# Optimization experiments

Measured on AMD Instinct MI355X. Metric: run time of the kernel, lower is better.

Reference implementation:

```python
import jax, jax.numpy as jnp
import numpy as np

NQ, NKV, D = 32, 8, 64
HID = 2048
EPS = 1e-5
THETA = 1000000.0


def _rmsnorm(x, w):
    var = jnp.mean(x * x, axis=-1, keepdims=True)
    return x * jax.lax.rsqrt(var + EPS) * w


def setup_inputs() -> dict:
    key = jax.random.key(0)
    k1, k2, k3 = jax.random.split(key, 3)
    T = 2048
    positions = jnp.arange(T, dtype=jnp.int64) if jax.config.jax_enable_x64 else jnp.arange(T, dtype=jnp.int32)
    hidden_states = jax.random.normal(k1, (T, HID), dtype=jnp.float32)
    w_qkv = jax.random.normal(k2, (HID, (NQ + 2 * NKV) * D), dtype=jnp.float32) / np.sqrt(HID)
    w_out = jax.random.normal(k3, (NQ * D, HID), dtype=jnp.float32) / np.sqrt(NQ * D)
    q_ln_w = jnp.ones((D,), dtype=jnp.float32)
    k_ln_w = jnp.ones((D,), dtype=jnp.float32)
    return {"positions": positions, "hidden_states": hidden_states, "w_qkv": w_qkv,
            "w_out": w_out, "q_ln_w": q_ln_w, "k_ln_w": k_ln_w}


def reference(positions, hidden_states, w_qkv, w_out, q_ln_w, k_ln_w):
    T = hidden_states.shape[0]
    qkv = hidden_states @ w_qkv  # [T, (NQ+2*NKV)*D]
    q = qkv[:, : NQ * D].reshape(T, NQ, D)
    k = qkv[:, NQ * D : (NQ + NKV) * D].reshape(T, NKV, D)
    v = qkv[:, (NQ + NKV) * D :].reshape(T, NKV, D)
    # per-head RMSNorm on q and k
    q = _rmsnorm(q, q_ln_w)
    k = _rmsnorm(k, k_ln_w)
    # neox-style RoPE (rotate halves)
    inv_freq = 1.0 / (THETA ** (jnp.arange(0, D, 2, dtype=jnp.float32) / D))
    ang = positions.astype(jnp.float32)[:, None] * inv_freq  # [T, D/2]
    cos = jnp.cos(ang)[:, None, :]
    sin = jnp.sin(ang)[:, None, :]
    def rope(x):
        x1, x2 = x[..., : D // 2], x[..., D // 2 :]
        return jnp.concatenate([x1 * cos - x2 * sin, x2 * cos + x1 * sin], axis=-1)
    q = rope(q)
    k = rope(k)
    # grouped-query causal attention (one sequence, positions define order)
    G = NQ // NKV
    qg = q.reshape(T, NKV, G, D)
    scores = jnp.einsum('tkgd,skd->kgts', qg, k) * (D ** -0.5)  # [NKV,G,T,T]
    causal = jnp.arange(T)[:, None] >= jnp.arange(T)[None, :]
    scores = jnp.where(causal[None, None], scores, -1e30)
    probs = jax.nn.softmax(scores, axis=-1)
    attn = jnp.einsum('kgts,skd->tkgd', probs, v).reshape(T, NQ * D)
    return attn @ w_out
```

## Files before the change

kernel.cpp:

```cpp
#include <hip/hip_runtime.h>

typedef __bf16 bhalf;
typedef __bf16 bhalf8 __attribute__((ext_vector_type(8)));
typedef __bf16 bhalf4 __attribute__((ext_vector_type(4)));
typedef float f32x4 __attribute__((ext_vector_type(4)));

typedef __attribute__((address_space(1))) const void* gas_p;
typedef __attribute__((address_space(3))) void* las_p;

#define T_SEQ 2048
#define HIDN  2048
#define NQH   32
#define NKVH  8
#define DH    64
#define NQKV  3072

__global__ __launch_bounds__(256) void cast_bf16_k(const float* __restrict__ in,
                                                   bhalf* __restrict__ out, int n) {
  int i = (blockIdx.x * 256 + threadIdx.x) * 4;
  if (i + 3 < n) {
    float4 v = *(const float4*)(in + i);
    bhalf4 o;
    o[0] = (bhalf)v.x; o[1] = (bhalf)v.y; o[2] = (bhalf)v.z; o[3] = (bhalf)v.w;
    *(bhalf4*)(out + i) = o;
  }
}

__global__ __launch_bounds__(256) void transpose_cast_k(const float* __restrict__ in,
                                                        bhalf* __restrict__ out, int R, int C) {
  __shared__ float tile[32][33];
  int bx = blockIdx.x * 32;
  int by = blockIdx.y * 32;
  int tx = threadIdx.x & 31, ty = threadIdx.x >> 5;
#pragma unroll
  for (int p = 0; p < 4; ++p)
    tile[ty + 8 * p][tx] = in[(size_t)(by + ty + 8 * p) * C + bx + tx];
  __syncthreads();
#pragma unroll
  for (int p = 0; p < 4; ++p)
    out[(size_t)(bx + ty + 8 * p) * R + by + tx] = (bhalf)tile[tx][ty + 8 * p];
}

__global__ __launch_bounds__(256) void transpose_bf16_k(const bhalf* __restrict__ in,
                                                        bhalf* __restrict__ out, int R, int C) {
  __shared__ bhalf tile[32][33];
  int bx = blockIdx.x * 32;
  int by = blockIdx.y * 32;
  int tx = threadIdx.x & 31, ty = threadIdx.x >> 5;
#pragma unroll
  for (int p = 0; p < 4; ++p)
    tile[ty + 8 * p][tx] = in[(size_t)(by + ty + 8 * p) * C + bx + tx];
  __syncthreads();
#pragma unroll
  for (int p = 0; p < 4; ++p)
    out[(size_t)(bx + ty + 8 * p) * R + by + tx] = tile[tx][ty + 8 * p];
}

__device__ __forceinline__ void gemm_core(const bhalf* __restrict__ A,
                                          const bhalf* __restrict__ Bt, int K,
                                          int bm, int bn, int tid,
                                          bhalf* As, bhalf* Bs, f32x4 acc[2][4]) {
  int lane = tid & 63, wv = tid >> 6;
  int m16 = lane & 15, q4 = lane >> 4;
  int srow = tid >> 3;
  int scol = ((tid & 7) ^ (srow & 7)) * 8;
  const bhalf* asrc = A + (size_t)(bm + srow) * K + scol;
  const bhalf* bsrc = Bt + (size_t)(bn + srow) * K + scol;
  bhalf* adst = As + (wv * 8) * 64;
  bhalf* bdst = Bs + (wv * 8) * 64;
  int swz = m16 & 7;

  for (int k0 = 0; k0 < K; k0 += 64) {
#pragma unroll
    for (int c = 0; c < 4; ++c)
      __builtin_amdgcn_global_load_lds((gas_p)(asrc + (size_t)(c * 32) * K + k0),
                                       (las_p)(adst + c * 2048), 16, 0, 0);
#pragma unroll
    for (int c = 0; c < 2; ++c)
      __builtin_amdgcn_global_load_lds((gas_p)(bsrc + (size_t)(c * 32) * K + k0),
                                       (las_p)(bdst + c * 2048), 16, 0, 0);
    __syncthreads();
    bhalf8 af[2][2], bf[4][2];
#pragma unroll
    for (int mi = 0; mi < 2; ++mi)
#pragma unroll
      for (int ks = 0; ks < 2; ++ks)
        af[mi][ks] = *(const bhalf8*)&As[(wv * 32 + mi * 16 + m16) * 64 +
                                         (((ks * 4 + q4) ^ swz) * 8)];
#pragma unroll
    for (int ni = 0; ni < 4; ++ni)
#pragma unroll
      for (int ks = 0; ks < 2; ++ks)
        bf[ni][ks] = *(const bhalf8*)&Bs[(ni * 16 + m16) * 64 +
                                         (((ks * 4 + q4) ^ swz) * 8)];
#pragma unroll
    for (int mi = 0; mi < 2; ++mi)
#pragma unroll
      for (int ni = 0; ni < 4; ++ni) {
        acc[mi][ni] = __builtin_amdgcn_mfma_f32_16x16x32_bf16(af[mi][0], bf[ni][0], acc[mi][ni], 0, 0, 0);
        acc[mi][ni] = __builtin_amdgcn_mfma_f32_16x16x32_bf16(af[mi][1], bf[ni][1], acc[mi][ni], 0, 0, 0);
      }
    __syncthreads();
  }
}

__global__ __launch_bounds__(256) void gemm1_fused_k(const bhalf* __restrict__ A,
                                                     const bhalf* __restrict__ Bt,
                                                     const int* __restrict__ pos,
                                                     const float* __restrict__ qw,
                                                     const float* __restrict__ kw,
                                                     bhalf* __restrict__ qo,
                                                     bhalf* __restrict__ ko,
                                                     bhalf* __restrict__ vo) {
  __shared__ __align__(16) bhalf As[128 * 64];
  __shared__ __align__(16) bhalf Bs[64 * 64];
  int tid = threadIdx.x, lane = tid & 63, wv = tid >> 6;
  int m16 = lane & 15, q4 = lane >> 4;
  int bm = blockIdx.y * 128, bn = blockIdx.x * 64, h = blockIdx.x;
  f32x4 zero4 = {0.f, 0.f, 0.f, 0.f};
  f32x4 acc[2][4];
#pragma unroll
  for (int mi = 0; mi < 2; ++mi)
#pragma unroll
    for (int ni = 0; ni < 4; ++ni) acc[mi][ni] = zero4;

  gemm_core(A, Bt, HIDN, bm, bn, tid, As, Bs, acc);

  int wr0 = wv * 32;
  if (h < 40) {
    float wd[4];
    const float* wptr = (h < 32) ? qw : kw;
#pragma unroll
    for (int ni = 0; ni < 4; ++ni) wd[ni] = wptr[ni * 16 + m16];
    float f0 = exp2f((float)m16 * -0.6228615177913804f);
    float f1 = f0 * 0.001f;
#pragma unroll
    for (int mi = 0; mi < 2; ++mi)
#pragma unroll
      for (int r = 0; r < 4; ++r) {
        int trow = bm + wr0 + mi * 16 + q4 * 4 + r;
        float x0 = acc[mi][0][r], x1 = acc[mi][1][r], x2 = acc[mi][2][r], x3 = acc[mi][3][r];
        float ss = x0 * x0 + x1 * x1 + x2 * x2 + x3 * x3;
        ss += __shfl_xor(ss, 1);
        ss += __shfl_xor(ss, 2);
        ss += __shfl_xor(ss, 4);
        ss += __shfl_xor(ss, 8);
        float sc = rsqrtf(ss * (1.0f / 64.0f) + 1e-5f);
        float y0 = x0 * sc * wd[0], y1 = x1 * sc * wd[1];
        float y2 = x2 * sc * wd[2], y3 = x3 * sc * wd[3];
        float p = (float)pos[trow];
        float a0 = p * f0, a1 = p * f1;
        float c0 = cosf(a0), s0 = sinf(a0), c1 = cosf(a1), s1 = sinf(a1);
        float o0 = y0 * c0 - y2 * s0, o2 = y2 * c0 + y0 * s0;
        float o1 = y1 * c1 - y3 * s1, o3 = y3 * c1 + y1 * s1;
        bhalf* dst = (h < 32) ? (qo + (size_t)trow * 2048 + h * 64 + m16)
                              : (ko + (size_t)trow * 512 + (h - 32) * 64 + m16);
        dst[0] = (bhalf)o0; dst[16] = (bhalf)o1; dst[32] = (bhalf)o2; dst[48] = (bhalf)o3;
      }
  } else {
#pragma unroll
    for (int mi = 0; mi < 2; ++mi)
#pragma unroll
      for (int r = 0; r < 4; ++r) {
        int trow = bm + wr0 + mi * 16 + q4 * 4 + r;
        bhalf* dst = vo + (size_t)trow * 512 + (h - 40) * 64 + m16;
        dst[0] = (bhalf)acc[mi][0][r]; dst[16] = (bhalf)acc[mi][1][r];
        dst[32] = (bhalf)acc[mi][2][r]; dst[48] = (bhalf)acc[mi][3][r];
      }
  }
}

__global__ __launch_bounds__(256) void gemm2_k(const bhalf* __restrict__ A,
                                               const bhalf* __restrict__ Bt,
                                               float* __restrict__ C) {
  __shared__ __align__(16) bhalf As[128 * 64];
  __shared__ __align__(16) bhalf Bs[64 * 64];
  int tid = threadIdx.x, lane = tid & 63, wv = tid >> 6;
  int m16 = lane & 15, q4 = lane >> 4;
  int bm = blockIdx.y * 128, bn = blockIdx.x * 64;
  f32x4 zero4 = {0.f, 0.f, 0.f, 0.f};
  f32x4 acc[2][4];
#pragma unroll
  for (int mi = 0; mi < 2; ++mi)
#pragma unroll
    for (int ni = 0; ni < 4; ++ni) acc[mi][ni] = zero4;

  gemm_core(A, Bt, HIDN, bm, bn, tid, As, Bs, acc);

  int wr0 = wv * 32;
#pragma unroll
  for (int mi = 0; mi < 2; ++mi)
#pragma unroll
    for (int r = 0; r < 4; ++r) {
      size_t base = (size_t)(bm + wr0 + mi * 16 + q4 * 4 + r) * 2048 + bn + m16;
      C[base] = acc[mi][0][r]; C[base + 16] = acc[mi][1][r];
      C[base + 32] = acc[mi][2][r]; C[base + 48] = acc[mi][3][r];
    }
}

__global__ __launch_bounds__(256) void attn_k(const bhalf* __restrict__ q,
                                              const bhalf* __restrict__ k,
                                              const bhalf* __restrict__ vt,
                                              bhalf* __restrict__ o) {
  __shared__ __align__(16) bhalf Kb[2][4096];
  __shared__ __align__(16) bhalf Vb[2][4096];
  __shared__ __align__(16) bhalf Pb[4][16][72];
  int tid = threadIdx.x, lane = tid & 63, w = tid >> 6;
  int h = blockIdx.x, kh = h >> 2;
  int qt = 31 - blockIdx.y;
  int qb = qt * 64;
  int m16 = lane & 15, q4 = lane >> 4;
  int wrow0 = qb + w * 16;

  const float C1 = 0.18033688011112042f;
  const float C2 = 11.541560327111707f;

  const bhalf* qp = q + (size_t)(wrow0 + m16) * 2048 + h * 64;
  bhalf8 qf0 = *(const bhalf8*)(qp + q4 * 8);
  bhalf8 qf1 = *(const bhalf8*)(qp + 32 + q4 * 8);

  int srow = tid >> 3;
  int scol = ((tid & 7) ^ (srow & 7)) * 8;
  const bhalf* ksrc = k + (size_t)srow * 512 + kh * 64 + scol;
  const bhalf* vsrc = vt + (size_t)(kh * 64 + srow) * 2048 + scol;
  bhalf* kdst = &Kb[0][0] + w * 512;
  bhalf* vdst = &Vb[0][0] + w * 512;

  auto stage = [&](int c) {
    int buf = c & 1, s0 = c * 64;
#pragma unroll
    for (int j = 0; j < 2; ++j) {
      __builtin_amdgcn_global_load_lds((gas_p)(ksrc + (size_t)(s0 + j * 32) * 512),
                                       (las_p)(kdst + buf * 4096 + j * 2048), 16, 0, 0);
      __builtin_amdgcn_global_load_lds((gas_p)(vsrc + (size_t)(j * 32) * 2048 + s0),
                                       (las_p)(vdst + buf * 4096 + j * 2048), 16, 0, 0);
    }
  };

  f32x4 zero4 = {0.f, 0.f, 0.f, 0.f};
  f32x4 oac[4];
  float psum[4] = {0.f, 0.f, 0.f, 0.f};
#pragma unroll
  for (int ni = 0; ni < 4; ++ni) oac[ni] = zero4;
  int swz = m16 & 7;

  stage(0);
  for (int c = 0; c <= qt; ++c) {
    __syncthreads();
    if (c < qt) stage(c + 1);
    int buf = c & 1, s0 = c * 64;
    if (c < qt) {
      bhalf8 kf[4][2];
#pragma unroll
      for (int st = 0; st < 4; ++st)
#pragma unroll
        for (int ks = 0; ks < 2; ++ks)
          kf[st][ks] = *(const bhalf8*)&Kb[buf][(st * 16 + m16) * 64 + (((ks * 4 + q4) ^ swz) * 8)];
      f32x4 sv[4];
#pragma unroll
      for (int st = 0; st < 4; ++st) {
        f32x4 t0 = __builtin_amdgcn_mfma_f32_16x16x32_bf16(qf0, kf[st][0], zero4, 0, 0, 0);
        sv[st] = __builtin_amdgcn_mfma_f32_16x16x32_bf16(qf1, kf[st][1], t0, 0, 0, 0);
      }
#pragma unroll
      for (int st = 0; st < 4; ++st)
#pragma unroll
        for (int r = 0; r < 4; ++r) {
          float pe = exp2f(sv[st][r] * C1 - C2);
          psum[r] += pe;
          Pb[w][q4 * 4 + r][st * 16 + m16] = (bhalf)pe;
        }
      bhalf8 vf[4][2];
#pragma unroll
      for (int ni = 0; ni < 4; ++ni)
#pragma unroll
        for (int ks = 0; ks < 2; ++ks)
          vf[ni][ks] = *(const bhalf8*)&Vb[buf][(ni * 16 + m16) * 64 + (((ks * 4 + q4) ^ swz) * 8)];
      bhalf8 ap0 = *(const bhalf8*)&Pb[w][m16][q4 * 8];
      bhalf8 ap1 = *(const bhalf8*)&Pb[w][m16][32 + q4 * 8];
#pragma unroll
      for (int ni = 0; ni < 4; ++ni) {
        oac[ni] = __builtin_amdgcn_mfma_f32_16x16x32_bf16(ap0, vf[ni][0], oac[ni], 0, 0, 0);
        oac[ni] = __builtin_amdgcn_mfma_f32_16x16x32_bf16(ap1, vf[ni][1], oac[ni], 0, 0, 0);
      }
    } else {
      bhalf8 kf[4][2];
      f32x4 sv[4];
#pragma unroll
      for (int st = 0; st < 4; ++st)
        if (st <= w) {
#pragma unroll
          for (int ks = 0; ks < 2; ++ks)
            kf[st][ks] = *(const bhalf8*)&Kb[buf][(st * 16 + m16) * 64 + (((ks * 4 + q4) ^ swz) * 8)];
          f32x4 t0 = __builtin_amdgcn_mfma_f32_16x16x32_bf16(qf0, kf[st][0], zero4, 0, 0, 0);
          sv[st] = __builtin_amdgcn_mfma_f32_16x16x32_bf16(qf1, kf[st][1], t0, 0, 0, 0);
        }
      int stwr = (w >= 2) ? 3 : 1;
#pragma unroll
      for (int st = 0; st < 4; ++st) {
        if (st > stwr) continue;
#pragma unroll
        for (int r = 0; r < 4; ++r) {
          float pe = 0.f;
          if (st <= w) {
            int trow = wrow0 + q4 * 4 + r;
            int col = s0 + st * 16 + m16;
            pe = (col <= trow) ? exp2f(sv[st][r] * C1 - C2) : 0.f;
          }
          psum[r] += pe;
          Pb[w][q4 * 4 + r][st * 16 + m16] = (bhalf)pe;
        }
      }
      int ksmax = (w >= 2) ? 1 : 0;
      bhalf8 vf[4][2];
#pragma unroll
      for (int ni = 0; ni < 4; ++ni)
#pragma unroll
        for (int ks = 0; ks < 2; ++ks)
          if (ks <= ksmax)
            vf[ni][ks] = *(const bhalf8*)&Vb[buf][(ni * 16 + m16) * 64 + (((ks * 4 + q4) ^ swz) * 8)];
      bhalf8 ap0 = *(const bhalf8*)&Pb[w][m16][q4 * 8];
#pragma unroll
      for (int ni = 0; ni < 4; ++ni)
        oac[ni] = __builtin_amdgcn_mfma_f32_16x16x32_bf16(ap0, vf[ni][0], oac[ni], 0, 0, 0);
      if (ksmax) {
        bhalf8 ap1 = *(const bhalf8*)&Pb[w][m16][32 + q4 * 8];
#pragma unroll
        for (int ni = 0; ni < 4; ++ni)
          oac[ni] = __builtin_amdgcn_mfma_f32_16x16x32_bf16(ap1, vf[ni][1], oac[ni], 0, 0, 0);
      }
    }
  }
#pragma unroll
  for (int r = 0; r < 4; ++r) {
    float ps = psum[r];
    ps += __shfl_xor(ps, 1);
    ps += __shfl_xor(ps, 2);
    ps += __shfl_xor(ps, 4);
    ps += __shfl_xor(ps, 8);
    psum[r] = 1.0f / ps;
  }
#pragma unroll
  for (int ni = 0; ni < 4; ++ni)
#pragma unroll
    for (int r = 0; r < 4; ++r) {
      int trow = wrow0 + q4 * 4 + r;
      o[(size_t)trow * 2048 + h * 64 + ni * 16 + m16] = (bhalf)(oac[ni][r] * psum[r]);
    }
}

extern "C" void kernel_launch(void* const* d_in, const int* in_sizes, int n_in,
                              void* d_out, int out_size, void* d_ws, size_t ws_size,
                              hipStream_t stream) {
  const int* positions = (const int*)d_in[0];
  const float* hidden  = (const float*)d_in[1];
  const float* w_qkv   = (const float*)d_in[2];
  const float* w_out   = (const float*)d_in[3];
  const float* q_ln    = (const float*)d_in[4];
  const float* k_ln    = (const float*)d_in[5];
  float* out = (float*)d_out;

  char* wsp = (char*)d_ws;
  bhalf* hid_bf  = (bhalf*)(wsp);
  bhalf* wqkvT   = (bhalf*)(wsp + 8388608);
  bhalf* woutT   = (bhalf*)(wsp + 20971520);
  bhalf* q_bf    = (bhalf*)(wsp + 29360128);
  bhalf* k_bf    = (bhalf*)(wsp + 37748736);
  bhalf* v_bf    = (bhalf*)(wsp + 39845888);
  bhalf* vt_g    = (bhalf*)(wsp + 41943040);
  bhalf* attn_bf = (bhalf*)(wsp + 44040192);

  cast_bf16_k<<<T_SEQ * HIDN / 1024, 256, 0, stream>>>(hidden, hid_bf, T_SEQ * HIDN);
  transpose_cast_k<<<dim3(NQKV / 32, HIDN / 32), 256, 0, stream>>>(w_qkv, wqkvT, HIDN, NQKV);
  transpose_cast_k<<<dim3(HIDN / 32, HIDN / 32), 256, 0, stream>>>(w_out, woutT, HIDN, HIDN);
  gemm1_fused_k<<<dim3(NQKV / 64, T_SEQ / 128), 256, 0, stream>>>(
      hid_bf, wqkvT, positions, q_ln, k_ln, q_bf, k_bf, v_bf);
  transpose_bf16_k<<<dim3(512 / 32, T_SEQ / 32), 256, 0, stream>>>(v_bf, vt_g, T_SEQ, 512);
  attn_k<<<dim3(NQH, 32), 256, 0, stream>>>(q_bf, k_bf, vt_g, attn_bf);
  gemm2_k<<<dim3(HIDN / 64, T_SEQ / 128), 256, 0, stream>>>(attn_bf, woutT, out);
}
```

Before: 222.7 us.

## Widen attention query tiles, split-K output GEMM, vectorize weight transpose-cast

The attention kernel now gives each block 128 query rows and each wave 32 rows in two MFMA row tiles, so every staged K/V chunk is reused across twice as many queries. The diagonal-chunk masking is recomputed for the new tiling, and the kernel gets a launch-bounds occupancy hint. The output projection GEMM is split into two K halves, which doubles the grid to fill more CUs, and a new elementwise kernel sums the two partial results, at the cost of extra fp32 traffic and one more launch. The weight transpose-casts now use 64x64 tiles with float4 loads and 16-byte bf16 stores, and the workspace layout is reshuffled so the partial buffers alias the dead inputs.

```diff
diff --git a/kernel.cpp b/kernel.cpp
--- a/kernel.cpp
+++ b/kernel.cpp
@@ -26,19 +26,28 @@
   }
 }
 
-__global__ __launch_bounds__(256) void transpose_cast_k(const float* __restrict__ in,
-                                                        bhalf* __restrict__ out, int R, int C) {
-  __shared__ float tile[32][33];
-  int bx = blockIdx.x * 32;
-  int by = blockIdx.y * 32;
-  int tx = threadIdx.x & 31, ty = threadIdx.x >> 5;
-#pragma unroll
-  for (int p = 0; p < 4; ++p)
-    tile[ty + 8 * p][tx] = in[(size_t)(by + ty + 8 * p) * C + bx + tx];
+__global__ __launch_bounds__(256) void transpose_cast64_k(const float* __restrict__ in,
+                                                          bhalf* __restrict__ out,
+                                                          int R, int C) {
+  __shared__ bhalf tile[64][72];
+  int tid = threadIdx.x;
+  int bx = blockIdx.x * 64;
+  int by = blockIdx.y * 64;
+  int rl = tid >> 4, c4 = (tid & 15) * 4;
+#pragma unroll
+  for (int p = 0; p < 4; ++p) {
+    float4 v = *(const float4*)(in + (size_t)(by + rl + 16 * p) * C + bx + c4);
+    bhalf4 b;
+    b[0] = (bhalf)v.x; b[1] = (bhalf)v.y; b[2] = (bhalf)v.z; b[3] = (bhalf)v.w;
+    *(bhalf4*)&tile[rl + 16 * p][c4] = b;
+  }
   __syncthreads();
-#pragma unroll
-  for (int p = 0; p < 4; ++p)
-    out[(size_t)(bx + ty + 8 * p) * R + by + tx] = (bhalf)tile[tx][ty + 8 * p];
+  int c = tid >> 2, r0 = (tid & 3) * 16;
+  bhalf8 o0, o1;
+#pragma unroll
+  for (int j = 0; j < 8; ++j) { o0[j] = tile[r0 + j][c]; o1[j] = tile[r0 + 8 + j][c]; }
+  *(bhalf8*)(out + (size_t)(bx + c) * R + by + r0) = o0;
+  *(bhalf8*)(out + (size_t)(bx + c) * R + by + r0 + 8) = o1;
 }
 
 __global__ __launch_bounds__(256) void transpose_bf16_k(const bhalf* __restrict__ in,
@@ -57,27 +66,28 @@
 }
 
 __device__ __forceinline__ void gemm_core(const bhalf* __restrict__ A,
-                                          const bhalf* __restrict__ Bt, int K,
+                                          const bhalf* __restrict__ Bt,
+                                          int Kstride, int Klen,
                                           int bm, int bn, int tid,
                                           bhalf* As, bhalf* Bs, f32x4 acc[2][4]) {
   int lane = tid & 63, wv = tid >> 6;
   int m16 = lane & 15, q4 = lane >> 4;
   int srow = tid >> 3;
   int scol = ((tid & 7) ^ (srow & 7)) * 8;
-  const bhalf* asrc = A + (size_t)(bm + srow) * K + scol;
-  const bhalf* bsrc = Bt + (size_t)(bn + srow) * K + scol;
+  const bhalf* asrc = A + (size_t)(bm + srow) * Kstride + scol;
+  const bhalf* bsrc = Bt + (size_t)(bn + srow) * Kstride + scol;
   bhalf* adst = As + (wv * 8) * 64;
   bhalf* bdst = Bs + (wv * 8) * 64;
   int swz = m16 & 7;
 
-  for (int k0 = 0; k0 < K; k0 += 64) {
+  for (int k0 = 0; k0 < Klen; k0 += 64) {
 #pragma unroll
     for (int c = 0; c < 4; ++c)
-      __builtin_amdgcn_global_load_lds((gas_p)(asrc + (size_t)(c * 32) * K + k0),
+      __builtin_amdgcn_global_load_lds((gas_p)(asrc + (size_t)(c * 32) * Kstride + k0),
                                        (las_p)(adst + c * 2048), 16, 0, 0);
 #pragma unroll
     for (int c = 0; c < 2; ++c)
-      __builtin_amdgcn_global_load_lds((gas_p)(bsrc + (size_t)(c * 32) * K + k0),
+      __builtin_amdgcn_global_load_lds((gas_p)(bsrc + (size_t)(c * 32) * Kstride + k0),
                                        (las_p)(bdst + c * 2048), 16, 0, 0);
     __syncthreads();
     bhalf8 af[2][2], bf[4][2];
@@ -124,7 +134,7 @@
 #pragma unroll
     for (int ni = 0; ni < 4; ++ni) acc[mi][ni] = zero4;
 
-  gemm_core(A, Bt, HIDN, bm, bn, tid, As, Bs, acc);
+  gemm_core(A, Bt, HIDN, HIDN, bm, bn, tid, As, Bs, acc);
 
   int wr0 = wv * 32;
   if (h < 40) {
@@ -172,12 +182,13 @@
 
 __global__ __launch_bounds__(256) void gemm2_k(const bhalf* __restrict__ A,
                                                const bhalf* __restrict__ Bt,
-                                               float* __restrict__ C) {
+                                               float* __restrict__ Cpart) {
   __shared__ __align__(16) bhalf As[128 * 64];
   __shared__ __align__(16) bhalf Bs[64 * 64];
   int tid = threadIdx.x, lane = tid & 63, wv = tid >> 6;
   int m16 = lane & 15, q4 = lane >> 4;
   int bm = blockIdx.y * 128, bn = blockIdx.x * 64;
+  int slice = blockIdx.z;
   f32x4 zero4 = {0.f, 0.f, 0.f, 0.f};
   f32x4 acc[2][4];
 #pragma unroll
@@ -185,8 +196,9 @@
 #pragma unroll
     for (int ni = 0; ni < 4; ++ni) acc[mi][ni] = zero4;
 
-  gemm_core(A, Bt, HIDN, bm, bn, tid, As, Bs, acc);
-
+  gemm_core(A + slice * 1024, Bt + slice * 1024, HIDN, 1024, bm, bn, tid, As, Bs, acc);
+
+  float* C = Cpart + (size_t)slice * (T_SEQ * HIDN);
   int wr0 = wv * 32;
 #pragma unroll
   for (int mi = 0; mi < 2; ++mi)
@@ -198,26 +210,43 @@
     }
 }
 
-__global__ __launch_bounds__(256) void attn_k(const bhalf* __restrict__ q,
-                                              const bhalf* __restrict__ k,
-                                              const bhalf* __restrict__ vt,
-                                              bhalf* __restrict__ o) {
+__global__ __launch_bounds__(256) void add2_k(const float* __restrict__ p0,
+                                              const float* __restrict__ p1,
+                                              float* __restrict__ out) {
+  int i = (blockIdx.x * 256 + threadIdx.x) * 4;
+  float4 a = *(const float4*)(p0 + i);
+  float4 b = *(const float4*)(p1 + i);
+  float4 o = {a.x + b.x, a.y + b.y, a.z + b.z, a.w + b.w};
+  *(float4*)(out + i) = o;
+}
+
+__global__ __launch_bounds__(256, 3) void attn_k(const bhalf* __restrict__ q,
+                                                 const bhalf* __restrict__ k,
+                                                 const bhalf* __restrict__ vt,
+                                                 bhalf* __restrict__ o) {
   __shared__ __align__(16) bhalf Kb[2][4096];
   __shared__ __align__(16) bhalf Vb[2][4096];
-  __shared__ __align__(16) bhalf Pb[4][16][72];
+  __shared__ __align__(16) bhalf Pb[4][32][72];
   int tid = threadIdx.x, lane = tid & 63, w = tid >> 6;
   int h = blockIdx.x, kh = h >> 2;
-  int qt = 31 - blockIdx.y;
-  int qb = qt * 64;
+  int qt = 15 - blockIdx.y;
+  int qb = qt * 128;
   int m16 = lane & 15, q4 = lane >> 4;
-  int wrow0 = qb + w * 16;
+  int wrow0 = qb + w * 32;
+  int dw = w & 1;
+  int c_d = wrow0 >> 6;
+  int nch = 2 * qt + 2;
 
   const float C1 = 0.18033688011112042f;
   const float C2 = 11.541560327111707f;
 
-  const bhalf* qp = q + (size_t)(wrow0 + m16) * 2048 + h * 64;
-  bhalf8 qf0 = *(const bhalf8*)(qp + q4 * 8);
-  bhalf8 qf1 = *(const bhalf8*)(qp + 32 + q4 * 8);
+  bhalf8 qf[2][2];
+#pragma unroll
+  for (int mt = 0; mt < 2; ++mt) {
+    const bhalf* qp = q + (size_t)(wrow0 + mt * 16 + m16) * 2048 + h * 64;
+    qf[mt][0] = *(const bhalf8*)(qp + q4 * 8);
+    qf[mt][1] = *(const bhalf8*)(qp + 32 + q4 * 8);
+  }
 
   int srow = tid >> 3;
   int scol = ((tid & 7) ^ (srow & 7)) * 8;
@@ -238,115 +267,138 @@
   };
 
   f32x4 zero4 = {0.f, 0.f, 0.f, 0.f};
-  f32x4 oac[4];
-  float psum[4] = {0.f, 0.f, 0.f, 0.f};
-#pragma unroll
-  for (int ni = 0; ni < 4; ++ni) oac[ni] = zero4;
+  f32x4 oac[2][4];
+  float psum[2][4];
+#pragma unroll
+  for (int mt = 0; mt < 2; ++mt)
+#pragma unroll
+    for (int ni = 0; ni < 4; ++ni) oac[mt][ni] = zero4;
+#pragma unroll
+  for (int mt = 0; mt < 2; ++mt)
+#pragma unroll
+    for (int r = 0; r < 4; ++r) psum[mt][r] = 0.f;
   int swz = m16 & 7;
 
   stage(0);
-  for (int c = 0; c <= qt; ++c) {
+  for (int c = 0; c < nch; ++c) {
     __syncthreads();
-    if (c < qt) stage(c + 1);
-    int buf = c & 1, s0 = c * 64;
-    if (c < qt) {
+    if (c + 1 < nch) stage(c + 1);
+    if (c > c_d) continue;
+    int buf = c & 1;
+    if (c < c_d) {
       bhalf8 kf[4][2];
 #pragma unroll
       for (int st = 0; st < 4; ++st)
 #pragma unroll
         for (int ks = 0; ks < 2; ++ks)
           kf[st][ks] = *(const bhalf8*)&Kb[buf][(st * 16 + m16) * 64 + (((ks * 4 + q4) ^ swz) * 8)];
-      f32x4 sv[4];
-#pragma unroll
-      for (int st = 0; st < 4; ++st) {
-        f32x4 t0 = __builtin_amdgcn_mfma_f32_16x16x32_bf16(qf0, kf[st][0], zero4, 0, 0, 0);
-        sv[st] = __builtin_amdgcn_mfma_f32_16x16x32_bf16(qf1, kf[st][1], t0, 0, 0, 0);
-      }
-#pragma unroll
-      for (int st = 0; st < 4; ++st)
-#pragma unroll
-        for (int r = 0; r < 4; ++r) {
-          float pe = exp2f(sv[st][r] * C1 - C2);
-          psum[r] += pe;
-          Pb[w][q4 * 4 + r][st * 16 + m16] = (bhalf)pe;
+#pragma unroll
+      for (int mt = 0; mt < 2; ++mt) {
+        f32x4 sv[4];
+#pragma unroll
+        for (int st = 0; st < 4; ++st) {
+          f32x4 t0 = __builtin_amdgcn_mfma_f32_16x16x32_bf16(qf[mt][0], kf[st][0], zero4, 0, 0, 0);
+          sv[st] = __builtin_amdgcn_mfma_f32_16x16x32_bf16(qf[mt][1], kf[st][1], t0, 0, 0, 0);
         }
+#pragma unroll
+        for (int st = 0; st < 4; ++st)
+#pragma unroll
+          for (int r = 0; r < 4; ++r) {
+            float pe = exp2f(sv[st][r] * C1 - C2);
+            psum[mt][r] += pe;
+            Pb[w][mt * 16 + q4 * 4 + r][st * 16 + m16] = (bhalf)pe;
+          }
+      }
       bhalf8 vf[4][2];
 #pragma unroll
       for (int ni = 0; ni < 4; ++ni)
 #pragma unroll
         for (int ks = 0; ks < 2; ++ks)
           vf[ni][ks] = *(const bhalf8*)&Vb[buf][(ni * 16 + m16) * 64 + (((ks * 4 + q4) ^ swz) * 8)];
-      bhalf8 ap0 = *(const bhalf8*)&Pb[w][m16][q4 * 8];
-      bhalf8 ap1 = *(const bhalf8*)&Pb[w][m16][32 + q4 * 8];
-#pragma unroll
-      for (int ni = 0; ni < 4; ++ni) {
-        oac[ni] = __builtin_amdgcn_mfma_f32_16x16x32_bf16(ap0, vf[ni][0], oac[ni], 0, 0, 0);
-        oac[ni] = __builtin_amdgcn_mfma_f32_16x16x32_bf16(ap1, vf[ni][1], oac[ni], 0, 0, 0);
+#pragma unroll
+      for (int mt = 0; mt < 2; ++mt) {
+        bhalf8 ap0 = *(const bhalf8*)&Pb[w][mt * 16 + m16][q4 * 8];
+        bhalf8 ap1 = *(const bhalf8*)&Pb[w][mt * 16 + m16][32 + q4 * 8];
+#pragma unroll
+        for (int ni = 0; ni < 4; ++ni) {
+          oac[mt][ni] = __builtin_amdgcn_mfma_f32_16x16x32_bf16(ap0, vf[ni][0], oac[mt][ni], 0, 0, 0);
+          oac[mt][ni] = __builtin_amdgcn_mfma_f32_16x16x32_bf16(ap1, vf[ni][1], oac[mt][ni], 0, 0, 0);
+        }
       }
     } else {
+      int stwr = 1 + 2 * dw;
       bhalf8 kf[4][2];
-      f32x4 sv[4];
 #pragma unroll
       for (int st = 0; st < 4; ++st)
-        if (st <= w) {
+        if (st <= stwr)
 #pragma unroll
           for (int ks = 0; ks < 2; ++ks)
             kf[st][ks] = *(const bhalf8*)&Kb[buf][(st * 16 + m16) * 64 + (((ks * 4 + q4) ^ swz) * 8)];
-          f32x4 t0 = __builtin_amdgcn_mfma_f32_16x16x32_bf16(qf0, kf[st][0], zero4, 0, 0, 0);
-          sv[st] = __builtin_amdgcn_mfma_f32_16x16x32_bf16(qf1, kf[st][1], t0, 0, 0, 0);
+#pragma unroll
+      for (int mt = 0; mt < 2; ++mt) {
+        f32x4 sv[4];
+#pragma unroll
+        for (int st = 0; st < 4; ++st)
+          if (st <= mt + 2 * dw) {
+            f32x4 t0 = __builtin_amdgcn_mfma_f32_16x16x32_bf16(qf[mt][0], kf[st][0], zero4, 0, 0, 0);
+            sv[st] = __builtin_amdgcn_mfma_f32_16x16x32_bf16(qf[mt][1], kf[st][1], t0, 0, 0, 0);
+          }
+#pragma unroll
+        for (int st = 0; st < 4; ++st) {
+          if (st > stwr) continue;
+          int d = st - 2 * dw - mt;
+#pragma unroll
+          for (int r = 0; r < 4; ++r) {
+            float pe = 0.f;
+            if (d < 0) pe = exp2f(sv[st][r] * C1 - C2);
+            else if (d == 0) pe = (m16 <= q4 * 4 + r) ? exp2f(sv[st][r] * C1 - C2) : 0.f;
+            psum[mt][r] += pe;
+            Pb[w][mt * 16 + q4 * 4 + r][st * 16 + m16] = (bhalf)pe;
+          }
         }
-      int stwr = (w >= 2) ? 3 : 1;
-#pragma unroll
-      for (int st = 0; st < 4; ++st) {
-        if (st > stwr) continue;
-#pragma unroll
-        for (int r = 0; r < 4; ++r) {
-          float pe = 0.f;
-          if (st <= w) {
-            int trow = wrow0 + q4 * 4 + r;
-            int col = s0 + st * 16 + m16;
-            pe = (col <= trow) ? exp2f(sv[st][r] * C1 - C2) : 0.f;
-          }
-          psum[r] += pe;
-          Pb[w][q4 * 4 + r][st * 16 + m16] = (bhalf)pe;
+      }
+      bhalf8 vf[4][2];
+#pragma unroll
+      for (int ni = 0; ni < 4; ++ni) {
+        vf[ni][0] = *(const bhalf8*)&Vb[buf][(ni * 16 + m16) * 64 + ((q4 ^ swz) * 8)];
+        if (dw)
+          vf[ni][1] = *(const bhalf8*)&Vb[buf][(ni * 16 + m16) * 64 + (((4 + q4) ^ swz) * 8)];
+      }
+#pragma unroll
+      for (int mt = 0; mt < 2; ++mt) {
+        bhalf8 ap0 = *(const bhalf8*)&Pb[w][mt * 16 + m16][q4 * 8];
+#pragma unroll
+        for (int ni = 0; ni < 4; ++ni)
+          oac[mt][ni] = __builtin_amdgcn_mfma_f32_16x16x32_bf16(ap0, vf[ni][0], oac[mt][ni], 0, 0, 0);
+        if (dw) {
+          bhalf8 ap1 = *(const bhalf8*)&Pb[w][mt * 16 + m16][32 + q4 * 8];
+#pragma unroll
+          for (int ni = 0; ni < 4; ++ni)
+            oac[mt][ni] = __builtin_amdgcn_mfma_f32_16x16x32_bf16(ap1, vf[ni][1], oac[mt][ni], 0, 0, 0);
         }
       }
-      int ksmax = (w >= 2) ? 1 : 0;
-      bhalf8 vf[4][2];
-#pragma unroll
-      for (int ni = 0; ni < 4; ++ni)
-#pragma unroll
-        for (int ks = 0; ks < 2; ++ks)
-          if (ks <= ksmax)
-            vf[ni][ks] = *(const bhalf8*)&Vb[buf][(ni * 16 + m16) * 64 + (((ks * 4 + q4) ^ swz) * 8)];
-      bhalf8 ap0 = *(const bhalf8*)&Pb[w][m16][q4 * 8];
-#pragma unroll
-      for (int ni = 0; ni < 4; ++ni)
-        oac[ni] = __builtin_amdgcn_mfma_f32_16x16x32_bf16(ap0, vf[ni][0], oac[ni], 0, 0, 0);
-      if (ksmax) {
-        bhalf8 ap1 = *(const bhalf8*)&Pb[w][m16][32 + q4 * 8];
-#pragma unroll
-        for (int ni = 0; ni < 4; ++ni)
-          oac[ni] = __builtin_amdgcn_mfma_f32_16x16x32_bf16(ap1, vf[ni][1], oac[ni], 0, 0, 0);
-      }
     }
   }
 #pragma unroll
-  for (int r = 0; r < 4; ++r) {
-    float ps = psum[r];
-    ps += __shfl_xor(ps, 1);
-    ps += __shfl_xor(ps, 2);
-    ps += __shfl_xor(ps, 4);
-    ps += __shfl_xor(ps, 8);
-    psum[r] = 1.0f / ps;
-  }
-#pragma unroll
-  for (int ni = 0; ni < 4; ++ni)
+  for (int mt = 0; mt < 2; ++mt)
 #pragma unroll
     for (int r = 0; r < 4; ++r) {
-      int trow = wrow0 + q4 * 4 + r;
-      o[(size_t)trow * 2048 + h * 64 + ni * 16 + m16] = (bhalf)(oac[ni][r] * psum[r]);
+      float ps = psum[mt][r];
+      ps += __shfl_xor(ps, 1);
+      ps += __shfl_xor(ps, 2);
+      ps += __shfl_xor(ps, 4);
+      ps += __shfl_xor(ps, 8);
+      psum[mt][r] = 1.0f / ps;
     }
+#pragma unroll
+  for (int mt = 0; mt < 2; ++mt)
+#pragma unroll
+    for (int ni = 0; ni < 4; ++ni)
+#pragma unroll
+      for (int r = 0; r < 4; ++r) {
+        int trow = wrow0 + mt * 16 + q4 * 4 + r;
+        o[(size_t)trow * 2048 + h * 64 + ni * 16 + m16] = (bhalf)(oac[mt][ni][r] * psum[mt][r]);
+      }
 }
 
 extern "C" void kernel_launch(void* const* d_in, const int* in_sizes, int n_in,
@@ -361,21 +413,24 @@
   float* out = (float*)d_out;
 
   char* wsp = (char*)d_ws;
-  bhalf* hid_bf  = (bhalf*)(wsp);
-  bhalf* wqkvT   = (bhalf*)(wsp + 8388608);
-  bhalf* woutT   = (bhalf*)(wsp + 20971520);
-  bhalf* q_bf    = (bhalf*)(wsp + 29360128);
-  bhalf* k_bf    = (bhalf*)(wsp + 37748736);
-  bhalf* v_bf    = (bhalf*)(wsp + 39845888);
-  bhalf* vt_g    = (bhalf*)(wsp + 41943040);
-  bhalf* attn_bf = (bhalf*)(wsp + 44040192);
+  bhalf* woutT   = (bhalf*)(wsp);
+  bhalf* attn_bf = (bhalf*)(wsp + 8388608);
+  float* part0   = (float*)(wsp + 16777216);
+  float* part1   = (float*)(wsp + 33554432);
+  bhalf* hid_bf  = (bhalf*)(wsp + 16777216);
+  bhalf* wqkvT   = (bhalf*)(wsp + 25165824);
+  bhalf* q_bf    = (bhalf*)(wsp + 50331648);
+  bhalf* k_bf    = (bhalf*)(wsp + 58720256);
+  bhalf* v_bf    = (bhalf*)(wsp + 60817408);
+  bhalf* vt_g    = (bhalf*)(wsp + 62914560);
 
   cast_bf16_k<<<T_SEQ * HIDN / 1024, 256, 0, stream>>>(hidden, hid_bf, T_SEQ * HIDN);
-  transpose_cast_k<<<dim3(NQKV / 32, HIDN / 32), 256, 0, stream>>>(w_qkv, wqkvT, HIDN, NQKV);
-  transpose_cast_k<<<dim3(HIDN / 32, HIDN / 32), 256, 0, stream>>>(w_out, woutT, HIDN, HIDN);
+  transpose_cast64_k<<<dim3(NQKV / 64, HIDN / 64), 256, 0, stream>>>(w_qkv, wqkvT, HIDN, NQKV);
+  transpose_cast64_k<<<dim3(HIDN / 64, HIDN / 64), 256, 0, stream>>>(w_out, woutT, HIDN, HIDN);
   gemm1_fused_k<<<dim3(NQKV / 64, T_SEQ / 128), 256, 0, stream>>>(
       hid_bf, wqkvT, positions, q_ln, k_ln, q_bf, k_bf, v_bf);
   transpose_bf16_k<<<dim3(512 / 32, T_SEQ / 32), 256, 0, stream>>>(v_bf, vt_g, T_SEQ, 512);
-  attn_k<<<dim3(NQH, 32), 256, 0, stream>>>(q_bf, k_bf, vt_g, attn_bf);
-  gemm2_k<<<dim3(HIDN / 64, T_SEQ / 128), 256, 0, stream>>>(attn_bf, woutT, out);
-}
+  attn_k<<<dim3(NQH, 16), 256, 0, stream>>>(q_bf, k_bf, vt_g, attn_bf);
+  gemm2_k<<<dim3(HIDN / 64, T_SEQ / 128, 2), 256, 0, stream>>>(attn_bf, woutT, part0);
+  add2_k<<<T_SEQ * HIDN / 1024, 256, 0, stream>>>(part0, part1, out);
+}
```

Result: slower. 237.6 us (+6.7%).

## Shrink GEMM tiles, split-K output GEMM, fuse V transpose, vectorize weight transpose

Applied to the files above, without the earlier changes.

GEMM tiles shrink from 128x64 to 64x64 so more blocks are launched on the many-CU GPU. The output GEMM becomes a two-way split-K that writes two fp32 partial buffers, followed by an add kernel. The QKV GEMM epilogue now writes V already transposed, which removes the separate transpose kernel. The weight transpose-cast moves to 64x64 tiles with float4 loads and 16-byte stores. The cost is less data reuse per tile, extra fp32 partial-buffer traffic plus an extra launch, and strided 2-byte scattered stores for the transposed V.

```diff
diff --git a/kernel.cpp b/kernel.cpp
--- a/kernel.cpp
+++ b/kernel.cpp
@@ -26,80 +26,68 @@
   }
 }
 
-__global__ __launch_bounds__(256) void transpose_cast_k(const float* __restrict__ in,
-                                                        bhalf* __restrict__ out, int R, int C) {
-  __shared__ float tile[32][33];
-  int bx = blockIdx.x * 32;
-  int by = blockIdx.y * 32;
-  int tx = threadIdx.x & 31, ty = threadIdx.x >> 5;
-#pragma unroll
-  for (int p = 0; p < 4; ++p)
-    tile[ty + 8 * p][tx] = in[(size_t)(by + ty + 8 * p) * C + bx + tx];
+__global__ __launch_bounds__(256) void transpose_cast64_k(const float* __restrict__ in,
+                                                          bhalf* __restrict__ out,
+                                                          int R, int C) {
+  __shared__ bhalf tile[64][72];
+  int tid = threadIdx.x;
+  int bx = blockIdx.x * 64;
+  int by = blockIdx.y * 64;
+  int rl = tid >> 4, c4 = (tid & 15) * 4;
+#pragma unroll
+  for (int p = 0; p < 4; ++p) {
+    float4 v = *(const float4*)(in + (size_t)(by + rl + 16 * p) * C + bx + c4);
+    bhalf4 b;
+    b[0] = (bhalf)v.x; b[1] = (bhalf)v.y; b[2] = (bhalf)v.z; b[3] = (bhalf)v.w;
+    *(bhalf4*)&tile[rl + 16 * p][c4] = b;
+  }
   __syncthreads();
-#pragma unroll
-  for (int p = 0; p < 4; ++p)
-    out[(size_t)(bx + ty + 8 * p) * R + by + tx] = (bhalf)tile[tx][ty + 8 * p];
-}
-
-__global__ __launch_bounds__(256) void transpose_bf16_k(const bhalf* __restrict__ in,
-                                                        bhalf* __restrict__ out, int R, int C) {
-  __shared__ bhalf tile[32][33];
-  int bx = blockIdx.x * 32;
-  int by = blockIdx.y * 32;
-  int tx = threadIdx.x & 31, ty = threadIdx.x >> 5;
-#pragma unroll
-  for (int p = 0; p < 4; ++p)
-    tile[ty + 8 * p][tx] = in[(size_t)(by + ty + 8 * p) * C + bx + tx];
-  __syncthreads();
-#pragma unroll
-  for (int p = 0; p < 4; ++p)
-    out[(size_t)(bx + ty + 8 * p) * R + by + tx] = tile[tx][ty + 8 * p];
-}
-
-__device__ __forceinline__ void gemm_core(const bhalf* __restrict__ A,
-                                          const bhalf* __restrict__ Bt, int K,
-                                          int bm, int bn, int tid,
-                                          bhalf* As, bhalf* Bs, f32x4 acc[2][4]) {
+  int c = tid >> 2, r0 = (tid & 3) * 16;
+  bhalf8 o0, o1;
+#pragma unroll
+  for (int j = 0; j < 8; ++j) { o0[j] = tile[r0 + j][c]; o1[j] = tile[r0 + 8 + j][c]; }
+  *(bhalf8*)(out + (size_t)(bx + c) * R + by + r0) = o0;
+  *(bhalf8*)(out + (size_t)(bx + c) * R + by + r0 + 8) = o1;
+}
+
+__device__ __forceinline__ void gemm_core64(const bhalf* __restrict__ A,
+                                            const bhalf* __restrict__ Bt,
+                                            int Kstride, int Klen,
+                                            int bm, int bn, int tid,
+                                            bhalf* As, bhalf* Bs, f32x4 acc[4]) {
   int lane = tid & 63, wv = tid >> 6;
   int m16 = lane & 15, q4 = lane >> 4;
   int srow = tid >> 3;
   int scol = ((tid & 7) ^ (srow & 7)) * 8;
-  const bhalf* asrc = A + (size_t)(bm + srow) * K + scol;
-  const bhalf* bsrc = Bt + (size_t)(bn + srow) * K + scol;
+  const bhalf* asrc = A + (size_t)(bm + srow) * Kstride + scol;
+  const bhalf* bsrc = Bt + (size_t)(bn + srow) * Kstride + scol;
   bhalf* adst = As + (wv * 8) * 64;
   bhalf* bdst = Bs + (wv * 8) * 64;
   int swz = m16 & 7;
 
-  for (int k0 = 0; k0 < K; k0 += 64) {
-#pragma unroll
-    for (int c = 0; c < 4; ++c)
-      __builtin_amdgcn_global_load_lds((gas_p)(asrc + (size_t)(c * 32) * K + k0),
+  for (int k0 = 0; k0 < Klen; k0 += 64) {
+#pragma unroll
+    for (int c = 0; c < 2; ++c) {
+      __builtin_amdgcn_global_load_lds((gas_p)(asrc + (size_t)(c * 32) * Kstride + k0),
                                        (las_p)(adst + c * 2048), 16, 0, 0);
-#pragma unroll
-    for (int c = 0; c < 2; ++c)
-      __builtin_amdgcn_global_load_lds((gas_p)(bsrc + (size_t)(c * 32) * K + k0),
+      __builtin_amdgcn_global_load_lds((gas_p)(bsrc + (size_t)(c * 32) * Kstride + k0),
                                        (las_p)(bdst + c * 2048), 16, 0, 0);
+    }
     __syncthreads();
-    bhalf8 af[2][2], bf[4][2];
-#pragma unroll
-    for (int mi = 0; mi < 2; ++mi)
+    bhalf8 af[2], bf[4][2];
+#pragma unroll
+    for (int ks = 0; ks < 2; ++ks)
+      af[ks] = *(const bhalf8*)&As[(wv * 16 + m16) * 64 + (((ks * 4 + q4) ^ swz) * 8)];
+#pragma unroll
+    for (int ni = 0; ni < 4; ++ni)
 #pragma unroll
       for (int ks = 0; ks < 2; ++ks)
-        af[mi][ks] = *(const bhalf8*)&As[(wv * 32 + mi * 16 + m16) * 64 +
-                                         (((ks * 4 + q4) ^ swz) * 8)];
-#pragma unroll
-    for (int ni = 0; ni < 4; ++ni)
-#pragma unroll
-      for (int ks = 0; ks < 2; ++ks)
-        bf[ni][ks] = *(const bhalf8*)&Bs[(ni * 16 + m16) * 64 +
-                                         (((ks * 4 + q4) ^ swz) * 8)];
-#pragma unroll
-    for (int mi = 0; mi < 2; ++mi)
-#pragma unroll
-      for (int ni = 0; ni < 4; ++ni) {
-        acc[mi][ni] = __builtin_amdgcn_mfma_f32_16x16x32_bf16(af[mi][0], bf[ni][0], acc[mi][ni], 0, 0, 0);
-        acc[mi][ni] = __builtin_amdgcn_mfma_f32_16x16x32_bf16(af[mi][1], bf[ni][1], acc[mi][ni], 0, 0, 0);
-      }
+        bf[ni][ks] = *(const bhalf8*)&Bs[(ni * 16 + m16) * 64 + (((ks * 4 + q4) ^ swz) * 8)];
+#pragma unroll
+    for (int ni = 0; ni < 4; ++ni) {
+      acc[ni] = __builtin_amdgcn_mfma_f32_16x16x32_bf16(af[0], bf[ni][0], acc[ni], 0, 0, 0);
+      acc[ni] = __builtin_amdgcn_mfma_f32_16x16x32_bf16(af[1], bf[ni][1], acc[ni], 0, 0, 0);
+    }
     __syncthreads();
   }
 }
@@ -111,22 +99,19 @@
                                                      const float* __restrict__ kw,
                                                      bhalf* __restrict__ qo,
                                                      bhalf* __restrict__ ko,
-                                                     bhalf* __restrict__ vo) {
-  __shared__ __align__(16) bhalf As[128 * 64];
+                                                     bhalf* __restrict__ vt) {
+  __shared__ __align__(16) bhalf As[64 * 64];
   __shared__ __align__(16) bhalf Bs[64 * 64];
   int tid = threadIdx.x, lane = tid & 63, wv = tid >> 6;
   int m16 = lane & 15, q4 = lane >> 4;
-  int bm = blockIdx.y * 128, bn = blockIdx.x * 64, h = blockIdx.x;
+  int bm = blockIdx.y * 64, bn = blockIdx.x * 64, h = blockIdx.x;
   f32x4 zero4 = {0.f, 0.f, 0.f, 0.f};
-  f32x4 acc[2][4];
-#pragma unroll
-  for (int mi = 0; mi < 2; ++mi)
-#pragma unroll
-    for (int ni = 0; ni < 4; ++ni) acc[mi][ni] = zero4;
-
-  gemm_core(A, Bt, HIDN, bm, bn, tid, As, Bs, acc);
-
-  int wr0 = wv * 32;
+  f32x4 acc[4];
+#pragma unroll
+  for (int ni = 0; ni < 4; ++ni) acc[ni] = zero4;
+
+  gemm_core64(A, Bt, HIDN, HIDN, bm, bn, tid, As, Bs, acc);
+
   if (h < 40) {
     float wd[4];
     const float* wptr = (h < 32) ? qw : kw;
@@ -135,67 +120,70 @@
     float f0 = exp2f((float)m16 * -0.6228615177913804f);
     float f1 = f0 * 0.001f;
 #pragma unroll
-    for (int mi = 0; mi < 2; ++mi)
-#pragma unroll
-      for (int r = 0; r < 4; ++r) {
-        int trow = bm + wr0 + mi * 16 + q4 * 4 + r;
-        float x0 = acc[mi][0][r], x1 = acc[mi][1][r], x2 = acc[mi][2][r], x3 = acc[mi][3][r];
-        float ss = x0 * x0 + x1 * x1 + x2 * x2 + x3 * x3;
-        ss += __shfl_xor(ss, 1);
-        ss += __shfl_xor(ss, 2);
-        ss += __shfl_xor(ss, 4);
-        ss += __shfl_xor(ss, 8);
-        float sc = rsqrtf(ss * (1.0f / 64.0f) + 1e-5f);
-        float y0 = x0 * sc * wd[0], y1 = x1 * sc * wd[1];
-        float y2 = x2 * sc * wd[2], y3 = x3 * sc * wd[3];
-        float p = (float)pos[trow];
-        float a0 = p * f0, a1 = p * f1;
-        float c0 = cosf(a0), s0 = sinf(a0), c1 = cosf(a1), s1 = sinf(a1);
-        float o0 = y0 * c0 - y2 * s0, o2 = y2 * c0 + y0 * s0;
-        float o1 = y1 * c1 - y3 * s1, o3 = y3 * c1 + y1 * s1;
-        bhalf* dst = (h < 32) ? (qo + (size_t)trow * 2048 + h * 64 + m16)
-                              : (ko + (size_t)trow * 512 + (h - 32) * 64 + m16);
-        dst[0] = (bhalf)o0; dst[16] = (bhalf)o1; dst[32] = (bhalf)o2; dst[48] = (bhalf)o3;
-      }
+    for (int r = 0; r < 4; ++r) {
+      int trow = bm + wv * 16 + q4 * 4 + r;
+      float x0 = acc[0][r], x1 = acc[1][r], x2 = acc[2][r], x3 = acc[3][r];
+      float ss = x0 * x0 + x1 * x1 + x2 * x2 + x3 * x3;
+      ss += __shfl_xor(ss, 1);
+      ss += __shfl_xor(ss, 2);
+      ss += __shfl_xor(ss, 4);
+      ss += __shfl_xor(ss, 8);
+      float sc = rsqrtf(ss * (1.0f / 64.0f) + 1e-5f);
+      float y0 = x0 * sc * wd[0], y1 = x1 * sc * wd[1];
+      float y2 = x2 * sc * wd[2], y3 = x3 * sc * wd[3];
+      float p = (float)pos[trow];
+      float a0 = p * f0, a1 = p * f1;
+      float c0 = cosf(a0), s0 = sinf(a0), c1 = cosf(a1), s1 = sinf(a1);
+      float o0 = y0 * c0 - y2 * s0, o2 = y2 * c0 + y0 * s0;
+      float o1 = y1 * c1 - y3 * s1, o3 = y3 * c1 + y1 * s1;
+      bhalf* dst = (h < 32) ? (qo + (size_t)trow * 2048 + h * 64 + m16)
+                            : (ko + (size_t)trow * 512 + (h - 32) * 64 + m16);
+      dst[0] = (bhalf)o0; dst[16] = (bhalf)o1; dst[32] = (bhalf)o2; dst[48] = (bhalf)o3;
+    }
   } else {
 #pragma unroll
-    for (int mi = 0; mi < 2; ++mi)
-#pragma unroll
-      for (int r = 0; r < 4; ++r) {
-        int trow = bm + wr0 + mi * 16 + q4 * 4 + r;
-        bhalf* dst = vo + (size_t)trow * 512 + (h - 40) * 64 + m16;
-        dst[0] = (bhalf)acc[mi][0][r]; dst[16] = (bhalf)acc[mi][1][r];
-        dst[32] = (bhalf)acc[mi][2][r]; dst[48] = (bhalf)acc[mi][3][r];
-      }
+    for (int r = 0; r < 4; ++r) {
+      int trow = bm + wv * 16 + q4 * 4 + r;
+#pragma unroll
+      for (int ni = 0; ni < 4; ++ni)
+        vt[(size_t)((h - 40) * 64 + ni * 16 + m16) * 2048 + trow] = (bhalf)acc[ni][r];
+    }
   }
 }
 
 __global__ __launch_bounds__(256) void gemm2_k(const bhalf* __restrict__ A,
                                                const bhalf* __restrict__ Bt,
-                                               float* __restrict__ C) {
-  __shared__ __align__(16) bhalf As[128 * 64];
+                                               float* __restrict__ Cpart) {
+  __shared__ __align__(16) bhalf As[64 * 64];
   __shared__ __align__(16) bhalf Bs[64 * 64];
   int tid = threadIdx.x, lane = tid & 63, wv = tid >> 6;
   int m16 = lane & 15, q4 = lane >> 4;
-  int bm = blockIdx.y * 128, bn = blockIdx.x * 64;
+  int bm = blockIdx.y * 64, bn = blockIdx.x * 64;
+  int slice = blockIdx.z;
   f32x4 zero4 = {0.f, 0.f, 0.f, 0.f};
-  f32x4 acc[2][4];
-#pragma unroll
-  for (int mi = 0; mi < 2; ++mi)
-#pragma unroll
-    for (int ni = 0; ni < 4; ++ni) acc[mi][ni] = zero4;
-
-  gemm_core(A, Bt, HIDN, bm, bn, tid, As, Bs, acc);
-
-  int wr0 = wv * 32;
-#pragma unroll
-  for (int mi = 0; mi < 2; ++mi)
-#pragma unroll
-    for (int r = 0; r < 4; ++r) {
-      size_t base = (size_t)(bm + wr0 + mi * 16 + q4 * 4 + r) * 2048 + bn + m16;
-      C[base] = acc[mi][0][r]; C[base + 16] = acc[mi][1][r];
-      C[base + 32] = acc[mi][2][r]; C[base + 48] = acc[mi][3][r];
-    }
+  f32x4 acc[4];
+#pragma unroll
+  for (int ni = 0; ni < 4; ++ni) acc[ni] = zero4;
+
+  gemm_core64(A + slice * 1024, Bt + slice * 1024, HIDN, 1024, bm, bn, tid, As, Bs, acc);
+
+  float* C = Cpart + (size_t)slice * (T_SEQ * HIDN);
+#pragma unroll
+  for (int r = 0; r < 4; ++r) {
+    size_t base = (size_t)(bm + wv * 16 + q4 * 4 + r) * 2048 + bn + m16;
+    C[base] = acc[0][r]; C[base + 16] = acc[1][r];
+    C[base + 32] = acc[2][r]; C[base + 48] = acc[3][r];
+  }
+}
+
+__global__ __launch_bounds__(256) void add2_k(const float* __restrict__ p0,
+                                              const float* __restrict__ p1,
+                                              float* __restrict__ out) {
+  int i = (blockIdx.x * 256 + threadIdx.x) * 4;
+  float4 a = *(const float4*)(p0 + i);
+  float4 b = *(const float4*)(p1 + i);
+  float4 o = {a.x + b.x, a.y + b.y, a.z + b.z, a.w + b.w};
+  *(float4*)(out + i) = o;
 }
 
 __global__ __launch_bounds__(256) void attn_k(const bhalf* __restrict__ q,
@@ -361,21 +349,22 @@
   float* out = (float*)d_out;
 
   char* wsp = (char*)d_ws;
-  bhalf* hid_bf  = (bhalf*)(wsp);
-  bhalf* wqkvT   = (bhalf*)(wsp + 8388608);
-  bhalf* woutT   = (bhalf*)(wsp + 20971520);
-  bhalf* q_bf    = (bhalf*)(wsp + 29360128);
-  bhalf* k_bf    = (bhalf*)(wsp + 37748736);
-  bhalf* v_bf    = (bhalf*)(wsp + 39845888);
-  bhalf* vt_g    = (bhalf*)(wsp + 41943040);
-  bhalf* attn_bf = (bhalf*)(wsp + 44040192);
+  bhalf* woutT   = (bhalf*)(wsp);
+  bhalf* attn_bf = (bhalf*)(wsp + 8388608);
+  float* part0   = (float*)(wsp + 16777216);
+  float* part1   = (float*)(wsp + 33554432);
+  bhalf* hid_bf  = (bhalf*)(wsp + 16777216);
+  bhalf* wqkvT   = (bhalf*)(wsp + 25165824);
+  bhalf* q_bf    = (bhalf*)(wsp + 50331648);
+  bhalf* k_bf    = (bhalf*)(wsp + 58720256);
+  bhalf* vt_g    = (bhalf*)(wsp + 60817408);
 
   cast_bf16_k<<<T_SEQ * HIDN / 1024, 256, 0, stream>>>(hidden, hid_bf, T_SEQ * HIDN);
-  transpose_cast_k<<<dim3(NQKV / 32, HIDN / 32), 256, 0, stream>>>(w_qkv, wqkvT, HIDN, NQKV);
-  transpose_cast_k<<<dim3(HIDN / 32, HIDN / 32), 256, 0, stream>>>(w_out, woutT, HIDN, HIDN);
-  gemm1_fused_k<<<dim3(NQKV / 64, T_SEQ / 128), 256, 0, stream>>>(
-      hid_bf, wqkvT, positions, q_ln, k_ln, q_bf, k_bf, v_bf);
-  transpose_bf16_k<<<dim3(512 / 32, T_SEQ / 32), 256, 0, stream>>>(v_bf, vt_g, T_SEQ, 512);
+  transpose_cast64_k<<<dim3(NQKV / 64, HIDN / 64), 256, 0, stream>>>(w_qkv, wqkvT, HIDN, NQKV);
+  transpose_cast64_k<<<dim3(HIDN / 64, HIDN / 64), 256, 0, stream>>>(w_out, woutT, HIDN, HIDN);
+  gemm1_fused_k<<<dim3(NQKV / 64, T_SEQ / 64), 256, 0, stream>>>(
+      hid_bf, wqkvT, positions, q_ln, k_ln, q_bf, k_bf, vt_g);
   attn_k<<<dim3(NQH, 32), 256, 0, stream>>>(q_bf, k_bf, vt_g, attn_bf);
-  gemm2_k<<<dim3(HIDN / 64, T_SEQ / 128), 256, 0, stream>>>(attn_bf, woutT, out);
-}
+  gemm2_k<<<dim3(HIDN / 64, T_SEQ / 64, 2), 256, 0, stream>>>(attn_bf, woutT, part0);
+  add2_k<<<T_SEQ * HIDN / 1024, 256, 0, stream>>>(part0, part1, out);
+}
```

Result: slower. 237.9 us (+6.8%).
